# Kernel tuning notes

Measured on AMD Instinct MI355X. Metric: run time of the kernel, lower is better.

## Reference

```python
import jax, jax.numpy as jnp
import numpy as np

N_NODES = 50000
N_EDGES = 300000
HID = 256
IN_S, IN_D, IN_E, OUT = 10, 12, 3, 3
K = 2


def _mlp(x, W1, b1, W2, b2):
    # 2-layer MLP: Linear -> relu -> Linear (mlp_layers=2, activation='relu')
    h = jax.nn.relu(x @ W1 + b1)
    return h @ W2 + b2


def setup_inputs() -> dict:
    key = jax.random.key(0)
    ks = jax.random.split(key, 16)

    def w(k, shape):
        return (jax.random.normal(k, shape, jnp.float32) * 0.05)

    z = lambda n: jnp.zeros((n,), jnp.float32)
    return {
        "static_features": jax.random.normal(ks[0], (N_NODES, IN_S), jnp.float32),
        "dynamic_features": jax.random.normal(ks[1], (N_NODES, IN_D), jnp.float32),
        "edge_index": jax.random.randint(ks[2], (2, N_EDGES), 0, N_NODES),
        "edge_attr": jax.random.normal(ks[3], (N_EDGES, IN_E), jnp.float32),
        # static node encoder
        "sW1": w(ks[4], (IN_S, HID)), "sb1": z(HID), "sW2": w(ks[5], (HID, HID)), "sb2": z(HID),
        # dynamic node encoder
        "dW1": w(ks[6], (IN_D, HID)), "db1": z(HID), "dW2": w(ks[7], (HID, HID)), "db2": z(HID),
        # edge encoder (edge_mlp=True)
        "eW1": w(ks[8], (IN_E, HID)), "eb1": z(HID), "eW2": w(ks[9], (HID, HID)), "eb2": z(HID),
        # SWEGNN edge-weight MLP: input [e_ij, x_s_i, x_s_j] -> HID
        "gW1": w(ks[10], (3 * HID, HID)), "gb1": z(HID), "gW2": w(ks[11], (HID, HID)), "gb2": z(HID),
        # decoder
        "oW1": w(ks[12], (HID, HID)), "ob1": z(HID), "oW2": w(ks[13], (HID, OUT)), "ob2": z(OUT),
    }


def reference(static_features, dynamic_features, edge_index, edge_attr,
              sW1, sb1, sW2, sb2, dW1, db1, dW2, db2,
              eW1, eb1, eW2, eb2, gW1, gb1, gW2, gb2,
              oW1, ob1, oW2, ob2):
    # Encoders
    x_s = _mlp(static_features, sW1, sb1, sW2, sb2)   # [N, HID]
    x_d = _mlp(dynamic_features, dW1, db1, dW2, db2)  # [N, HID]
    e = _mlp(edge_attr, eW1, eb1, eW2, eb2)           # [E, HID]

    src, dst = edge_index[0], edge_index[1]

    # Edge-conditioned weights from edge feats + static embeddings of endpoints
    g_in = jnp.concatenate([e, x_s[src], x_s[dst]], axis=-1)  # [E, 3*HID]
    g = _mlp(g_in, gW1, gb1, gW2, gb2)                        # [E, HID]

    # Degree normalization (normalize=True)
    deg = jax.ops.segment_sum(jnp.ones((src.shape[0],), jnp.float32), dst,
                              num_segments=N_NODES)
    inv_deg = (1.0 / jnp.maximum(deg, 1.0))[:, None]  # [N, 1]

    # K hops of SWE message passing: m_ij = g_ij * (h_j - h_i)  (with_gradient=True)
    h = x_d
    for _ in range(K):
        m = g * (h[src] - h[dst])                                  # [E, HID]
        aggr = jax.ops.segment_sum(m, dst, num_segments=N_NODES)   # [N, HID]
        h = h + aggr * inv_deg                                     # residual update

    x = jnp.tanh(h)  # gnn_activation='tanh'
    return _mlp(x, oW1, ob1, oW2, ob2)  # [N, OUT]
```

## Files before the change

kernel.cpp:

```cpp
#include <hip/hip_runtime.h>
#include <hip/hip_bf16.h>

#define N_NODES 50000
#define N_EDGES 300000
#define HID 256
#define AS 264
#define A0S 40

typedef unsigned int uint;
typedef unsigned short ushort;
typedef short bf16x8 __attribute__((ext_vector_type(8)));
typedef unsigned short u16x8 __attribute__((ext_vector_type(8)));
typedef float f32x4 __attribute__((ext_vector_type(4)));

__device__ __forceinline__ float bf2f(ushort u){ union{uint i; float f;} v; v.i=((uint)u)<<16; return v.f; }
__device__ __forceinline__ ushort f2bf(float f){ __hip_bfloat16 h=__float2bfloat16(f); return *reinterpret_cast<ushort*>(&h); }

__device__ __forceinline__ f32x4 mfma16(bf16x8 a, bf16x8 b, f32x4 c){
    return __builtin_amdgcn_mfma_f32_16x16x32_bf16(a, b, c, 0, 0, 0);
}

__device__ __forceinline__ void wave_gemm(const ushort* act, const ushort* __restrict__ WT,
                                          int n0, int lane, f32x4 acc[4][4])
{
    #pragma unroll
    for (int mi=0;mi<4;mi++)
        #pragma unroll
        for (int ni=0;ni<4;ni++) acc[mi][ni]=(f32x4){0.f,0.f,0.f,0.f};
    const int rA=lane&15, kg=(lane>>4)*8;
    #pragma unroll
    for (int kk=0;kk<8;kk++){
        const int ka=kk*32+kg;
        bf16x8 a[4], b[4];
        #pragma unroll
        for (int mi=0;mi<4;mi++) a[mi]=*(const bf16x8*)&act[(mi*16+rA)*AS+ka];
        #pragma unroll
        for (int ni=0;ni<4;ni++) b[ni]=*(const bf16x8*)&WT[(size_t)((n0+ni*16+rA)*HID+ka)];
        #pragma unroll
        for (int mi=0;mi<4;mi++)
            #pragma unroll
            for (int ni=0;ni<4;ni++)
                acc[mi][ni]=mfma16(a[mi], b[ni], acc[mi][ni]);
    }
}

__device__ __forceinline__ void store_c_to_act(ushort* act, const f32x4 acc[4][4],
                                               int colb, int hi, bool relu)
{
    #pragma unroll
    for (int mi=0;mi<4;mi++)
        #pragma unroll
        for (int ni=0;ni<4;ni++)
            #pragma unroll
            for (int r=0;r<4;r++){
                float v=acc[mi][ni][r];
                if (relu) v=fmaxf(v,0.f);
                act[(mi*16+hi*4+r)*AS + colb+ni*16]=f2bf(v);
            }
}

__global__ void combine_weights(const float* __restrict__ sW2, const float* __restrict__ sb2,
                                const float* __restrict__ eW2, const float* __restrict__ eb2,
                                const float* __restrict__ gW1, const float* __restrict__ gb1,
                                const float* __restrict__ dW2, const float* __restrict__ gW2,
                                const float* __restrict__ oW1,
                                const float* __restrict__ eW1, const float* __restrict__ eb1,
                                const float* __restrict__ sW1, const float* __restrict__ sb1,
                                const float* __restrict__ dW1, const float* __restrict__ db1,
                                ushort* __restrict__ WT_A, ushort* __restrict__ WT_B, ushort* __restrict__ WT_E,
                                ushort* __restrict__ WT_d, ushort* __restrict__ WT_g, ushort* __restrict__ WT_o,
                                ushort* __restrict__ WT_e1, ushort* __restrict__ WT_s1, ushort* __restrict__ WT_d1,
                                float* __restrict__ bias_A, float* __restrict__ bias_B)
{
    const int j = threadIdx.x;
    const int i = blockIdx.x;
    const int m = blockIdx.y;
    if (m==6){ if (i<32) WT_e1[j*32+i] = f2bf(i<3 ? eW1[i*HID+j] : (i==3 ? eb1[j] : 0.f)); return; }
    if (m==7){ if (i<32) WT_s1[j*32+i] = f2bf(i<10? sW1[i*HID+j] : (i==10? sb1[j] : 0.f)); return; }
    if (m==8){ if (i<32) WT_d1[j*32+i] = f2bf(i<12? dW1[i*HID+j] : (i==12? db1[j] : 0.f)); return; }
    if (m>=3){
        if (i<HID){
            const float* S = (m==3)? dW2 : (m==4)? gW2 : oW1;
            ushort* D      = (m==3)? WT_d : (m==4)? WT_g : WT_o;
            D[j*HID+i]=f2bf(S[i*HID+j]);
        }
        return;
    }
    const float* L  = (m==2)? eW2 : sW2;
    const float* R  = gW1 + (m==0 ? HID*HID : (m==1 ? 2*HID*HID : 0));
    if (i < HID){
        float acc=0.f;
        for (int k=0;k<HID;k++) acc += L[i*HID+k]*R[k*HID+j];
        (m==0?WT_A:(m==1?WT_B:WT_E))[j*HID+i] = f2bf(acc);
    } else if (m==0){
        float acc=gb1[j];
        for (int k=0;k<HID;k++) acc += sb2[k]*gW1[(HID+k)*HID+j];
        for (int k=0;k<HID;k++) acc += eb2[k]*gW1[k*HID+j];
        bias_A[j]=acc;
    } else if (m==1){
        float acc=0.f;
        for (int k=0;k<HID;k++) acc += sb2[k]*gW1[(2*HID+k)*HID+j];
        bias_B[j]=acc;
    }
}

__global__ __launch_bounds__(256) void node_encode_mfma(
    const float* __restrict__ sfeat, const float* __restrict__ dfeat,
    const ushort* __restrict__ WT_s1, const ushort* __restrict__ WT_d1,
    const ushort* __restrict__ WT_d, const float* __restrict__ db2,
    const ushort* __restrict__ WT_A, const float* __restrict__ bias_A,
    const ushort* __restrict__ WT_B, const float* __restrict__ bias_B,
    ushort* __restrict__ gA, ushort* __restrict__ gB, ushort* __restrict__ h0)
{
    __shared__ ushort act[64*AS];
    __shared__ ushort A0[64*A0S];
    const int tid=threadIdx.x;
    const int n0blk=blockIdx.x*64;
    const int wv=tid>>6, lane=tid&63, n0=wv*64;
    const int rA=lane&15, kg=(lane>>4)*8, hi=lane>>4;
    const int colb=n0+rA;

    {
        const int n=tid>>2, k0=(tid&3)*8;
        const int gn=n0blk+n;
        u16x8 v;
        #pragma unroll
        for (int j=0;j<8;j++){
            const int k=k0+j;
            float f = (gn<N_NODES && k<10)? sfeat[(size_t)gn*10+k] : (k==10? 1.f : 0.f);
            v[j]=f2bf(f);
        }
        *(u16x8*)&A0[n*A0S+k0]=v;
    }
    __syncthreads();
    f32x4 acc[4][4];
    {
        bf16x8 a[4], b[4];
        #pragma unroll
        for (int mi=0;mi<4;mi++) a[mi]=*(const bf16x8*)&A0[(mi*16+rA)*A0S+kg];
        #pragma unroll
        for (int ni=0;ni<4;ni++) b[ni]=*(const bf16x8*)&WT_s1[(size_t)(n0+ni*16+rA)*32+kg];
        #pragma unroll
        for (int mi=0;mi<4;mi++)
            #pragma unroll
            for (int ni=0;ni<4;ni++)
                acc[mi][ni]=mfma16(a[mi], b[ni], (f32x4){0.f,0.f,0.f,0.f});
        store_c_to_act(act, acc, colb, hi, true);
    }
    __syncthreads();
    {
        const int n=tid>>2, k0=(tid&3)*8;
        const int gn=n0blk+n;
        u16x8 v;
        #pragma unroll
        for (int j=0;j<8;j++){
            const int k=k0+j;
            float f = (gn<N_NODES && k<12)? dfeat[(size_t)gn*12+k] : (k==12? 1.f : 0.f);
            v[j]=f2bf(f);
        }
        *(u16x8*)&A0[n*A0S+k0]=v;
    }
    {
        wave_gemm(act, WT_A, n0, lane, acc);
        #pragma unroll
        for (int mi=0;mi<4;mi++){
            #pragma unroll
            for (int ni=0;ni<4;ni++){
                const int col=colb+ni*16; const float bA=bias_A[col];
                #pragma unroll
                for (int r=0;r<4;r++){
                    int rr=mi*16+hi*4+r; int gn=n0blk+rr;
                    if (gn<N_NODES) gA[(size_t)gn*HID+col]=f2bf(acc[mi][ni][r]+bA);
                }
            }
        }
    }
    {
        wave_gemm(act, WT_B, n0, lane, acc);
        #pragma unroll
        for (int mi=0;mi<4;mi++){
            #pragma unroll
            for (int ni=0;ni<4;ni++){
                const int col=colb+ni*16; const float bB=bias_B[col];
                #pragma unroll
                for (int r=0;r<4;r++){
                    int rr=mi*16+hi*4+r; int gn=n0blk+rr;
                    if (gn<N_NODES) gB[(size_t)gn*HID+col]=f2bf(acc[mi][ni][r]+bB);
                }
            }
        }
    }
    __syncthreads();
    {
        bf16x8 a[4], b[4];
        #pragma unroll
        for (int mi=0;mi<4;mi++) a[mi]=*(const bf16x8*)&A0[(mi*16+rA)*A0S+kg];
        #pragma unroll
        for (int ni=0;ni<4;ni++) b[ni]=*(const bf16x8*)&WT_d1[(size_t)(n0+ni*16+rA)*32+kg];
        #pragma unroll
        for (int mi=0;mi<4;mi++)
            #pragma unroll
            for (int ni=0;ni<4;ni++)
                acc[mi][ni]=mfma16(a[mi], b[ni], (f32x4){0.f,0.f,0.f,0.f});
        store_c_to_act(act, acc, colb, hi, true);
    }
    __syncthreads();
    {
        wave_gemm(act, WT_d, n0, lane, acc);
        #pragma unroll
        for (int mi=0;mi<4;mi++){
            #pragma unroll
            for (int ni=0;ni<4;ni++){
                const int col=colb+ni*16; const float bo=db2[col];
                #pragma unroll
                for (int r=0;r<4;r++){
                    int rr=mi*16+hi*4+r; int gn=n0blk+rr;
                    if (gn<N_NODES) h0[(size_t)gn*HID+col]=f2bf(acc[mi][ni][r]+bo);
                }
            }
        }
    }
}

__global__ __launch_bounds__(512) void edge_encode_mfma(
    const float* __restrict__ eattr, const int* __restrict__ eidx,
    const int* __restrict__ csr_src, const int* __restrict__ csr_eid,
    const ushort* __restrict__ WT_e1,
    const ushort* __restrict__ WT_E,
    const ushort* __restrict__ WT_g2, const float* __restrict__ gb2,
    const ushort* __restrict__ gA, const ushort* __restrict__ gB,
    ushort* __restrict__ g_out)
{
    __shared__ ushort act[128*AS];
    __shared__ ushort A0[128*A0S];
    __shared__ int si[128], di[128], ei[128];
    const int tid=threadIdx.x;
    const int bid=blockIdx.x;
    const int s0=((bid&7)*293 + (bid>>3))*128;
    const int wv=tid>>6, lane=tid&63;
    const int wm=wv>>2, wn=wv&3;
    const int m0=wm*64, n0=wn*64;
    const int rA=lane&15, kg=(lane>>4)*8, hi=lane>>4;
    const int colb=n0+rA;

    if (tid<128){
        int s=s0+tid; bool v=s<N_EDGES;
        int eid=v? csr_eid[s]:0;
        si[tid]=v? csr_src[s]:0;
        di[tid]=v? eidx[N_EDGES+eid]:0;
        ei[tid]=eid;
    }
    __syncthreads();
    {
        const int n=tid>>2, k0=(tid&3)*8;
        const int eid=ei[n];
        u16x8 v;
        #pragma unroll
        for (int j=0;j<8;j++){
            const int k=k0+j;
            float f = (k<3)? eattr[(size_t)eid*3+k] : (k==3? 1.f : 0.f);
            v[j]=f2bf(f);
        }
        *(u16x8*)&A0[n*A0S+k0]=v;
    }
    __syncthreads();
    f32x4 acc[4][4];
    {
        bf16x8 a[4], b[4];
        #pragma unroll
        for (int mi=0;mi<4;mi++) a[mi]=*(const bf16x8*)&A0[(m0+mi*16+rA)*A0S+kg];
        #pragma unroll
        for (int ni=0;ni<4;ni++) b[ni]=*(const bf16x8*)&WT_e1[(size_t)(n0+ni*16+rA)*32+kg];
        #pragma unroll
        for (int mi=0;mi<4;mi++)
            #pragma unroll
            for (int ni=0;ni<4;ni++)
                acc[mi][ni]=mfma16(a[mi], b[ni], (f32x4){0.f,0.f,0.f,0.f});
        store_c_to_act(act + m0*AS, acc, colb, hi, true);
    }
    __syncthreads();
    wave_gemm(act + m0*AS, WT_E, n0, lane, acc);
    __syncthreads();
    store_c_to_act(act + m0*AS, acc, colb, hi, false);
    {
        const int row=m0+lane;
        const ushort* garow=&gA[(size_t)si[row]*HID + n0];
        const ushort* gbrow=&gB[(size_t)di[row]*HID + n0];
        ushort* arow=&act[row*AS + n0];
        #pragma unroll
        for (int j=0;j<8;j++){
            const int jb=((j+lane)&7)*8;
            u16x8 av=*(u16x8*)&arow[jb];
            u16x8 ga=*(const u16x8*)&garow[jb];
            u16x8 gb=*(const u16x8*)&gbrow[jb];
            u16x8 o;
            #pragma unroll
            for (int q=0;q<8;q++)
                o[q]=f2bf(fmaxf(bf2f(av[q])+bf2f(ga[q])+bf2f(gb[q]),0.f));
            *(u16x8*)&arow[jb]=o;
        }
    }
    __syncthreads();
    wave_gemm(act + m0*AS, WT_g2, n0, lane, acc);
    {
        #pragma unroll
        for (int mi=0;mi<4;mi++){
            #pragma unroll
            for (int ni=0;ni<4;ni++){
                const int col=colb+ni*16; const float bg=gb2[col];
                #pragma unroll
                for (int r=0;r<4;r++){
                    const int rr=m0+mi*16+hi*4+r;
                    if (s0+rr<N_EDGES)
                        g_out[(size_t)(s0+rr)*HID+col]=f2bf(acc[mi][ni][r]+bg);
                }
            }
        }
    }
}

__global__ void deg_count(const int* __restrict__ eidx, uint* __restrict__ deg){
    int e=blockIdx.x*blockDim.x+threadIdx.x;
    if (e<N_EDGES) atomicAdd(&deg[eidx[N_EDGES+e]],1u);
}

__global__ void scan_kernel(const uint* __restrict__ deg, uint* __restrict__ row_start){
    __shared__ uint wtot[16];
    __shared__ uint woff[17];
    __shared__ uint carry_s;
    const int tid=threadIdx.x, lane=tid&63, wid=tid>>6;
    if (tid==0) carry_s=0;
    __syncthreads();
    for (uint base=0; base<N_NODES; base+=1024){
        uint idx=base+tid;
        uint v=(idx<N_NODES)? deg[idx]:0u;
        uint s=v;
        #pragma unroll
        for (int d=1; d<64; d<<=1){
            uint t=__shfl_up(s,d,64);
            if (lane>=d) s+=t;
        }
        if (lane==63) wtot[wid]=s;
        __syncthreads();
        if (tid==0){ uint r=0; for (int i=0;i<16;i++){ woff[i]=r; r+=wtot[i]; } woff[16]=r; }
        __syncthreads();
        uint excl = carry_s + woff[wid] + s - v;
        if (idx<N_NODES) row_start[idx]=excl;
        __syncthreads();
        if (tid==0) carry_s += woff[16];
        __syncthreads();
    }
}

__global__ void csr_fill(const int* __restrict__ eidx, const uint* __restrict__ row_start,
                         uint* __restrict__ cursor, int* __restrict__ csr_src, int* __restrict__ csr_eid){
    int e=blockIdx.x*blockDim.x+threadIdx.x;
    if (e>=N_EDGES) return;
    int d=eidx[N_EDGES+e];
    uint pos=atomicAdd(&cursor[d],1u);
    uint s=row_start[d]+pos;
    csr_src[s]=eidx[e];
    csr_eid[s]=e;
}

__global__ __launch_bounds__(256) void hop_kernel(
    const ushort* __restrict__ h_in, ushort* __restrict__ h_out,
    const ushort* __restrict__ g, const int* __restrict__ csr_src,
    const uint* __restrict__ row_start, const uint* __restrict__ deg)
{
    const int gw=(blockIdx.x*blockDim.x+threadIdx.x)>>6;
    if (gw>=N_NODES) return;
    const int c0=(threadIdx.x&63)*4;
    ushort4 hd4=*(const ushort4*)&h_in[(size_t)gw*HID+c0];
    float4 hd; hd.x=bf2f(hd4.x); hd.y=bf2f(hd4.y); hd.z=bf2f(hd4.z); hd.w=bf2f(hd4.w);
    float4 acc=make_float4(0,0,0,0);
    const uint st=row_start[gw], len=deg[gw];
    for (uint u=0;u<len;u++){
        uint s=st+u;
        int sn=csr_src[s];
        ushort4 g4=*(const ushort4*)&g[(size_t)s*HID+c0];
        ushort4 hs4=*(const ushort4*)&h_in[(size_t)sn*HID+c0];
        acc.x += bf2f(g4.x)*(bf2f(hs4.x)-hd.x);
        acc.y += bf2f(g4.y)*(bf2f(hs4.y)-hd.y);
        acc.z += bf2f(g4.z)*(bf2f(hs4.z)-hd.z);
        acc.w += bf2f(g4.w)*(bf2f(hs4.w)-hd.w);
    }
    const float inv=1.f/fmaxf((float)len,1.f);
    ushort4 o; o.x=f2bf(hd.x+acc.x*inv); o.y=f2bf(hd.y+acc.y*inv);
               o.z=f2bf(hd.z+acc.z*inv); o.w=f2bf(hd.w+acc.w*inv);
    *(ushort4*)&h_out[(size_t)gw*HID+c0]=o;
}

__global__ __launch_bounds__(256) void decoder_mfma(
    const ushort* __restrict__ h, const ushort* __restrict__ WT_o,
    const float* __restrict__ ob1, const float* __restrict__ oW2, const float* __restrict__ ob2,
    float* __restrict__ out)
{
    __shared__ ushort act[64*AS];
    const int tid=threadIdx.x, n0blk=blockIdx.x*64;
    const int wv=tid>>6, lane=tid&63, n0=wv*64, colb=n0+(lane&15);
    {
        const int row=tid>>2, cc=(tid&3)*64;
        const int gn=n0blk+row;
        #pragma unroll
        for (int k=0;k<64;k+=8){
            u16x8 t;
            if (gn<N_NODES){
                u16x8 v=*(const u16x8*)&h[(size_t)gn*HID+cc+k];
                #pragma unroll
                for (int j=0;j<8;j++) t[j]=f2bf(tanhf(bf2f(v[j])));
            } else {
                #pragma unroll
                for (int j=0;j<8;j++) t[j]=0;
            }
            *(u16x8*)&act[row*AS+cc+k]=t;
        }
    }
    __syncthreads();
    f32x4 acc[4][4];
    wave_gemm(act, WT_o, n0, lane, acc);
    __syncthreads();
    #pragma unroll
    for (int mi=0;mi<4;mi++){
        #pragma unroll
        for (int ni=0;ni<4;ni++){
            const int col=colb+ni*16; const float b1=ob1[col];
            #pragma unroll
            for (int r=0;r<4;r++){
                const int rr=mi*16+(lane>>4)*4+r;
                act[rr*AS+col]=f2bf(fmaxf(acc[mi][ni][r]+b1,0.f));
            }
        }
    }
    __syncthreads();
    if (tid<192){
        const int n=tid/3, o=tid-n*3;
        float a=ob2[o];
        for (int k=0;k<HID;k++) a+=bf2f(act[n*AS+k])*oW2[k*3+o];
        const int gn=n0blk+n;
        if (gn<N_NODES) out[(size_t)gn*3+o]=a;
    }
}

extern "C" void kernel_launch(void* const* d_in, const int* in_sizes, int n_in,
                              void* d_out, int out_size, void* d_ws, size_t ws_size,
                              hipStream_t stream)
{
    (void)in_sizes; (void)n_in; (void)out_size;
    const float* sfeat=(const float*)d_in[0];
    const float* dfeat=(const float*)d_in[1];
    const int*   eidx =(const int*)  d_in[2];
    const float* eattr=(const float*)d_in[3];
    const float* sW1=(const float*)d_in[4];  const float* sb1=(const float*)d_in[5];
    const float* sW2=(const float*)d_in[6];  const float* sb2=(const float*)d_in[7];
    const float* dW1=(const float*)d_in[8];  const float* db1=(const float*)d_in[9];
    const float* dW2=(const float*)d_in[10]; const float* db2=(const float*)d_in[11];
    const float* eW1=(const float*)d_in[12]; const float* eb1=(const float*)d_in[13];
    const float* eW2=(const float*)d_in[14]; const float* eb2=(const float*)d_in[15];
    const float* gW1=(const float*)d_in[16]; const float* gb1=(const float*)d_in[17];
    const float* gW2=(const float*)d_in[18]; const float* gb2=(const float*)d_in[19];
    const float* oW1=(const float*)d_in[20]; const float* ob1=(const float*)d_in[21];
    const float* oW2=(const float*)d_in[22]; const float* ob2=(const float*)d_in[23];
    float* out=(float*)d_out;

    char* p=(char*)d_ws;
    size_t used=0;
    auto alloc=[&](size_t bytes)->char*{
        char* r=p+used; used += (bytes+255)&~(size_t)255; return r;
    };
    ushort* WT_A=(ushort*)alloc(HID*HID*2);
    ushort* WT_B=(ushort*)alloc(HID*HID*2);
    ushort* WT_E=(ushort*)alloc(HID*HID*2);
    ushort* WT_d=(ushort*)alloc(HID*HID*2);
    ushort* WT_g=(ushort*)alloc(HID*HID*2);
    ushort* WT_o=(ushort*)alloc(HID*HID*2);
    ushort* WT_e1=(ushort*)alloc(HID*32*2);
    ushort* WT_s1=(ushort*)alloc(HID*32*2);
    ushort* WT_d1=(ushort*)alloc(HID*32*2);
    float* bias_A=(float*)alloc(HID*4);
    float* bias_B=(float*)alloc(HID*4);
    ushort* gA=(ushort*)alloc((size_t)N_NODES*HID*2);
    ushort* gB=(ushort*)alloc((size_t)N_NODES*HID*2);
    ushort* g =(ushort*)alloc((size_t)N_EDGES*HID*2);
    ushort* h0=(ushort*)alloc((size_t)N_NODES*HID*2);
    uint* deg      =(uint*)alloc(N_NODES*4);
    uint* row_start=(uint*)alloc(N_NODES*4);
    uint* cursor   =(uint*)alloc(N_NODES*4);
    int* csr_src=(int*)alloc(N_EDGES*4);
    int* csr_eid=(int*)alloc(N_EDGES*4);
    ushort* h1=gA;

    if (used > ws_size) return;

    hipMemsetAsync(deg, 0, N_NODES*4, stream);
    hipMemsetAsync(cursor, 0, N_NODES*4, stream);

    combine_weights<<<dim3(HID+1,9),256,0,stream>>>(sW2,sb2,eW2,eb2,gW1,gb1,dW2,gW2,oW1,eW1,eb1,sW1,sb1,dW1,db1,
                                                    WT_A,WT_B,WT_E,WT_d,WT_g,WT_o,WT_e1,WT_s1,WT_d1,bias_A,bias_B);
    node_encode_mfma<<<(N_NODES+63)/64,256,0,stream>>>(sfeat,dfeat,WT_s1,WT_d1,WT_d,db2,WT_A,bias_A,WT_B,bias_B,gA,gB,h0);
    deg_count<<<(N_EDGES+255)/256,256,0,stream>>>(eidx,deg);
    scan_kernel<<<1,1024,0,stream>>>(deg,row_start);
    csr_fill<<<(N_EDGES+255)/256,256,0,stream>>>(eidx,row_start,cursor,csr_src,csr_eid);
    edge_encode_mfma<<<(N_EDGES+127)/128,512,0,stream>>>(eattr,eidx,csr_src,csr_eid,WT_e1,WT_E,WT_g,gb2,gA,gB,g);
    hop_kernel<<<N_NODES/4,256,0,stream>>>(h0,h1,g,csr_src,row_start,deg);
    hop_kernel<<<N_NODES/4,256,0,stream>>>(h1,h0,g,csr_src,row_start,deg);
    decoder_mfma<<<(N_NODES+63)/64,256,0,stream>>>(h0,WT_o,ob1,oW2,ob2,out);
}
```

Measured before the change: 581.0 us.

## Unroll hop gather, fuse tanh into hop, MFMA decoder output layer, vectorize scan

Several independent changes. The hop kernel now processes four neighbours per iteration with separate accumulators, which exposes more memory-level parallelism. The final hop applies tanh before storing, so the decoder no longer computes it. The decoder's scalar 256x3 output projection is replaced by an MFMA against a zero-padded 16-column weight tile. The scan also handles four elements per thread. The main risk is extra register pressure from the unrolled accumulators, and the MFMA output layer wastes most of its columns on padding.

```diff
diff --git a/kernel.cpp b/kernel.cpp
--- a/kernel.cpp
+++ b/kernel.cpp
@@ -67,9 +67,11 @@
                                 const float* __restrict__ eW1, const float* __restrict__ eb1,
                                 const float* __restrict__ sW1, const float* __restrict__ sb1,
                                 const float* __restrict__ dW1, const float* __restrict__ db1,
+                                const float* __restrict__ oW2,
                                 ushort* __restrict__ WT_A, ushort* __restrict__ WT_B, ushort* __restrict__ WT_E,
                                 ushort* __restrict__ WT_d, ushort* __restrict__ WT_g, ushort* __restrict__ WT_o,
                                 ushort* __restrict__ WT_e1, ushort* __restrict__ WT_s1, ushort* __restrict__ WT_d1,
+                                ushort* __restrict__ WT_o2p,
                                 float* __restrict__ bias_A, float* __restrict__ bias_B)
 {
     const int j = threadIdx.x;
@@ -78,6 +80,7 @@
     if (m==6){ if (i<32) WT_e1[j*32+i] = f2bf(i<3 ? eW1[i*HID+j] : (i==3 ? eb1[j] : 0.f)); return; }
     if (m==7){ if (i<32) WT_s1[j*32+i] = f2bf(i<10? sW1[i*HID+j] : (i==10? sb1[j] : 0.f)); return; }
     if (m==8){ if (i<32) WT_d1[j*32+i] = f2bf(i<12? dW1[i*HID+j] : (i==12? db1[j] : 0.f)); return; }
+    if (m==9){ if (i<16) WT_o2p[i*HID+j] = f2bf(i<3 ? oW2[j*3+i] : 0.f); return; }
     if (m>=3){
         if (i<HID){
             const float* S = (m==3)? dW2 : (m==4)? gW2 : oW1;
@@ -331,10 +334,14 @@
     const int tid=threadIdx.x, lane=tid&63, wid=tid>>6;
     if (tid==0) carry_s=0;
     __syncthreads();
-    for (uint base=0; base<N_NODES; base+=1024){
-        uint idx=base+tid;
-        uint v=(idx<N_NODES)? deg[idx]:0u;
-        uint s=v;
+    for (uint base=0; base<N_NODES; base+=4096){
+        uint idx=base+tid*4;
+        uint v0=(idx  <N_NODES)? deg[idx  ]:0u;
+        uint v1=(idx+1<N_NODES)? deg[idx+1]:0u;
+        uint v2=(idx+2<N_NODES)? deg[idx+2]:0u;
+        uint v3=(idx+3<N_NODES)? deg[idx+3]:0u;
+        uint s4=v0+v1+v2+v3;
+        uint s=s4;
         #pragma unroll
         for (int d=1; d<64; d<<=1){
             uint t=__shfl_up(s,d,64);
@@ -344,8 +351,11 @@
         __syncthreads();
         if (tid==0){ uint r=0; for (int i=0;i<16;i++){ woff[i]=r; r+=wtot[i]; } woff[16]=r; }
         __syncthreads();
-        uint excl = carry_s + woff[wid] + s - v;
-        if (idx<N_NODES) row_start[idx]=excl;
+        uint excl = carry_s + woff[wid] + s - s4;
+        if (idx  <N_NODES) row_start[idx  ]=excl;
+        if (idx+1<N_NODES) row_start[idx+1]=excl+v0;
+        if (idx+2<N_NODES) row_start[idx+2]=excl+v0+v1;
+        if (idx+3<N_NODES) row_start[idx+3]=excl+v0+v1+v2;
         __syncthreads();
         if (tid==0) carry_s += woff[16];
         __syncthreads();
@@ -363,6 +373,7 @@
     csr_eid[s]=e;
 }
 
+template<bool TANH>
 __global__ __launch_bounds__(256) void hop_kernel(
     const ushort* __restrict__ h_in, ushort* __restrict__ h_out,
     const ushort* __restrict__ g, const int* __restrict__ csr_src,
@@ -373,46 +384,65 @@
     const int c0=(threadIdx.x&63)*4;
     ushort4 hd4=*(const ushort4*)&h_in[(size_t)gw*HID+c0];
     float4 hd; hd.x=bf2f(hd4.x); hd.y=bf2f(hd4.y); hd.z=bf2f(hd4.z); hd.w=bf2f(hd4.w);
-    float4 acc=make_float4(0,0,0,0);
+    float4 a0=make_float4(0,0,0,0), a1=make_float4(0,0,0,0);
+    float4 a2=make_float4(0,0,0,0), a3=make_float4(0,0,0,0);
     const uint st=row_start[gw], len=deg[gw];
-    for (uint u=0;u<len;u++){
-        uint s=st+u;
-        int sn=csr_src[s];
-        ushort4 g4=*(const ushort4*)&g[(size_t)s*HID+c0];
-        ushort4 hs4=*(const ushort4*)&h_in[(size_t)sn*HID+c0];
-        acc.x += bf2f(g4.x)*(bf2f(hs4.x)-hd.x);
-        acc.y += bf2f(g4.y)*(bf2f(hs4.y)-hd.y);
-        acc.z += bf2f(g4.z)*(bf2f(hs4.z)-hd.z);
-        acc.w += bf2f(g4.w)*(bf2f(hs4.w)-hd.w);
+    uint u=0;
+    for (; u+4<=len; u+=4){
+        int n0=csr_src[st+u], n1=csr_src[st+u+1], n2=csr_src[st+u+2], n3=csr_src[st+u+3];
+        ushort4 g0=*(const ushort4*)&g[(size_t)(st+u  )*HID+c0];
+        ushort4 g1=*(const ushort4*)&g[(size_t)(st+u+1)*HID+c0];
+        ushort4 g2=*(const ushort4*)&g[(size_t)(st+u+2)*HID+c0];
+        ushort4 g3=*(const ushort4*)&g[(size_t)(st+u+3)*HID+c0];
+        ushort4 h0v=*(const ushort4*)&h_in[(size_t)n0*HID+c0];
+        ushort4 h1v=*(const ushort4*)&h_in[(size_t)n1*HID+c0];
+        ushort4 h2v=*(const ushort4*)&h_in[(size_t)n2*HID+c0];
+        ushort4 h3v=*(const ushort4*)&h_in[(size_t)n3*HID+c0];
+        a0.x+=bf2f(g0.x)*(bf2f(h0v.x)-hd.x); a0.y+=bf2f(g0.y)*(bf2f(h0v.y)-hd.y);
+        a0.z+=bf2f(g0.z)*(bf2f(h0v.z)-hd.z); a0.w+=bf2f(g0.w)*(bf2f(h0v.w)-hd.w);
+        a1.x+=bf2f(g1.x)*(bf2f(h1v.x)-hd.x); a1.y+=bf2f(g1.y)*(bf2f(h1v.y)-hd.y);
+        a1.z+=bf2f(g1.z)*(bf2f(h1v.z)-hd.z); a1.w+=bf2f(g1.w)*(bf2f(h1v.w)-hd.w);
+        a2.x+=bf2f(g2.x)*(bf2f(h2v.x)-hd.x); a2.y+=bf2f(g2.y)*(bf2f(h2v.y)-hd.y);
+        a2.z+=bf2f(g2.z)*(bf2f(h2v.z)-hd.z); a2.w+=bf2f(g2.w)*(bf2f(h2v.w)-hd.w);
+        a3.x+=bf2f(g3.x)*(bf2f(h3v.x)-hd.x); a3.y+=bf2f(g3.y)*(bf2f(h3v.y)-hd.y);
+        a3.z+=bf2f(g3.z)*(bf2f(h3v.z)-hd.z); a3.w+=bf2f(g3.w)*(bf2f(h3v.w)-hd.w);
+    }
+    for (; u<len; u++){
+        int n0=csr_src[st+u];
+        ushort4 g0=*(const ushort4*)&g[(size_t)(st+u)*HID+c0];
+        ushort4 h0v=*(const ushort4*)&h_in[(size_t)n0*HID+c0];
+        a0.x+=bf2f(g0.x)*(bf2f(h0v.x)-hd.x); a0.y+=bf2f(g0.y)*(bf2f(h0v.y)-hd.y);
+        a0.z+=bf2f(g0.z)*(bf2f(h0v.z)-hd.z); a0.w+=bf2f(g0.w)*(bf2f(h0v.w)-hd.w);
     }
     const float inv=1.f/fmaxf((float)len,1.f);
-    ushort4 o; o.x=f2bf(hd.x+acc.x*inv); o.y=f2bf(hd.y+acc.y*inv);
-               o.z=f2bf(hd.z+acc.z*inv); o.w=f2bf(hd.w+acc.w*inv);
+    float vx=hd.x+(a0.x+a1.x+a2.x+a3.x)*inv;
+    float vy=hd.y+(a0.y+a1.y+a2.y+a3.y)*inv;
+    float vz=hd.z+(a0.z+a1.z+a2.z+a3.z)*inv;
+    float vw=hd.w+(a0.w+a1.w+a2.w+a3.w)*inv;
+    if (TANH){ vx=tanhf(vx); vy=tanhf(vy); vz=tanhf(vz); vw=tanhf(vw); }
+    ushort4 o; o.x=f2bf(vx); o.y=f2bf(vy); o.z=f2bf(vz); o.w=f2bf(vw);
     *(ushort4*)&h_out[(size_t)gw*HID+c0]=o;
 }
 
 __global__ __launch_bounds__(256) void decoder_mfma(
-    const ushort* __restrict__ h, const ushort* __restrict__ WT_o,
-    const float* __restrict__ ob1, const float* __restrict__ oW2, const float* __restrict__ ob2,
+    const ushort* __restrict__ x, const ushort* __restrict__ WT_o,
+    const float* __restrict__ ob1, const ushort* __restrict__ WT_o2p, const float* __restrict__ ob2,
     float* __restrict__ out)
 {
     __shared__ ushort act[64*AS];
     const int tid=threadIdx.x, n0blk=blockIdx.x*64;
-    const int wv=tid>>6, lane=tid&63, n0=wv*64, colb=n0+(lane&15);
+    const int wv=tid>>6, lane=tid&63, n0=wv*64;
+    const int rA=lane&15, kg=(lane>>4)*8, hi=lane>>4;
+    const int colb=n0+rA;
     {
         const int row=tid>>2, cc=(tid&3)*64;
         const int gn=n0blk+row;
         #pragma unroll
         for (int k=0;k<64;k+=8){
             u16x8 t;
-            if (gn<N_NODES){
-                u16x8 v=*(const u16x8*)&h[(size_t)gn*HID+cc+k];
-                #pragma unroll
-                for (int j=0;j<8;j++) t[j]=f2bf(tanhf(bf2f(v[j])));
-            } else {
-                #pragma unroll
-                for (int j=0;j<8;j++) t[j]=0;
-            }
+            #pragma unroll
+            for (int j=0;j<8;j++) t[j]=0;
+            if (gn<N_NODES) t=*(const u16x8*)&x[(size_t)gn*HID+cc+k];
             *(u16x8*)&act[row*AS+cc+k]=t;
         }
     }
@@ -427,18 +457,31 @@
             const int col=colb+ni*16; const float b1=ob1[col];
             #pragma unroll
             for (int r=0;r<4;r++){
-                const int rr=mi*16+(lane>>4)*4+r;
+                const int rr=mi*16+hi*4+r;
                 act[rr*AS+col]=f2bf(fmaxf(acc[mi][ni][r]+b1,0.f));
             }
         }
     }
     __syncthreads();
-    if (tid<192){
-        const int n=tid/3, o=tid-n*3;
-        float a=ob2[o];
-        for (int k=0;k<HID;k++) a+=bf2f(act[n*AS+k])*oW2[k*3+o];
-        const int gn=n0blk+n;
-        if (gn<N_NODES) out[(size_t)gn*3+o]=a;
+    {
+        const int m0p=wv*16;
+        f32x4 a2=(f32x4){0.f,0.f,0.f,0.f};
+        #pragma unroll
+        for (int kk=0;kk<8;kk++){
+            const int ka=kk*32+kg;
+            bf16x8 a=*(const bf16x8*)&act[(m0p+rA)*AS+ka];
+            bf16x8 b=*(const bf16x8*)&WT_o2p[(size_t)rA*HID+ka];
+            a2=mfma16(a, b, a2);
+        }
+        const int col=rA;
+        if (col<3){
+            const float b2=ob2[col];
+            #pragma unroll
+            for (int r=0;r<4;r++){
+                const int gn=n0blk+m0p+hi*4+r;
+                if (gn<N_NODES) out[(size_t)gn*3+col]=a2[r]+b2;
+            }
+        }
     }
 }
 
@@ -477,6 +520,7 @@
     ushort* WT_e1=(ushort*)alloc(HID*32*2);
     ushort* WT_s1=(ushort*)alloc(HID*32*2);
     ushort* WT_d1=(ushort*)alloc(HID*32*2);
+    ushort* WT_o2p=(ushort*)alloc(16*HID*2);
     float* bias_A=(float*)alloc(HID*4);
     float* bias_B=(float*)alloc(HID*4);
     ushort* gA=(ushort*)alloc((size_t)N_NODES*HID*2);
@@ -495,14 +539,14 @@
     hipMemsetAsync(deg, 0, N_NODES*4, stream);
     hipMemsetAsync(cursor, 0, N_NODES*4, stream);
 
-    combine_weights<<<dim3(HID+1,9),256,0,stream>>>(sW2,sb2,eW2,eb2,gW1,gb1,dW2,gW2,oW1,eW1,eb1,sW1,sb1,dW1,db1,
-                                                    WT_A,WT_B,WT_E,WT_d,WT_g,WT_o,WT_e1,WT_s1,WT_d1,bias_A,bias_B);
+    combine_weights<<<dim3(HID+1,10),256,0,stream>>>(sW2,sb2,eW2,eb2,gW1,gb1,dW2,gW2,oW1,eW1,eb1,sW1,sb1,dW1,db1,oW2,
+                                                     WT_A,WT_B,WT_E,WT_d,WT_g,WT_o,WT_e1,WT_s1,WT_d1,WT_o2p,bias_A,bias_B);
     node_encode_mfma<<<(N_NODES+63)/64,256,0,stream>>>(sfeat,dfeat,WT_s1,WT_d1,WT_d,db2,WT_A,bias_A,WT_B,bias_B,gA,gB,h0);
     deg_count<<<(N_EDGES+255)/256,256,0,stream>>>(eidx,deg);
     scan_kernel<<<1,1024,0,stream>>>(deg,row_start);
     csr_fill<<<(N_EDGES+255)/256,256,0,stream>>>(eidx,row_start,cursor,csr_src,csr_eid);
     edge_encode_mfma<<<(N_EDGES+127)/128,512,0,stream>>>(eattr,eidx,csr_src,csr_eid,WT_e1,WT_E,WT_g,gb2,gA,gB,g);
-    hop_kernel<<<N_NODES/4,256,0,stream>>>(h0,h1,g,csr_src,row_start,deg);
-    hop_kernel<<<N_NODES/4,256,0,stream>>>(h1,h0,g,csr_src,row_start,deg);
-    decoder_mfma<<<(N_NODES+63)/64,256,0,stream>>>(h0,WT_o,ob1,oW2,ob2,out);
-}
+    hop_kernel<false><<<N_NODES/4,256,0,stream>>>(h0,h1,g,csr_src,row_start,deg);
+    hop_kernel<true ><<<N_NODES/4,256,0,stream>>>(h1,h0,g,csr_src,row_start,deg);
+    decoder_mfma<<<(N_NODES+63)/64,256,0,stream>>>(h0,WT_o,ob1,WT_o2p,ob2,out);
+}
```

New measurement: 532.4 us. -8.4%, faster.
